# Kernel optimization log

Hardware: AMD Instinct MI355X
Metric: run time of the kernel (lower is better)

## Reference

```python
import jax, jax.numpy as jnp
from jax import lax
import numpy as np

EPS = 1e-5  # BatchNorm eps


def setup_inputs() -> dict:
    key = jax.random.key(0)
    ks = jax.random.split(key, 4)
    T, B, C = 256, 128, 1024
    L, H, NCLS = 6, 1024, 1000
    x = jax.random.normal(ks[0], (T, B, C), dtype=jnp.float32)
    W = jax.random.normal(ks[1], (L, C, H), dtype=jnp.float32) * (1.0 / np.sqrt(C))
    b = jnp.zeros((L, H), dtype=jnp.float32)
    gamma = jnp.ones((L, H), dtype=jnp.float32)
    beta = jnp.zeros((L, H), dtype=jnp.float32)
    u = jax.random.uniform(ks[2], (L, H), dtype=jnp.float32)  # recurrent weights in (0, U_bound~1)
    Wc = jax.random.normal(ks[3], (H, NCLS), dtype=jnp.float32) * (1.0 / np.sqrt(H))
    bc = jnp.zeros((NCLS,), dtype=jnp.float32)
    return {"x": x, "W": W, "b": b, "gamma": gamma, "beta": beta, "u": u, "Wc": Wc, "bc": bc}


def _layer(h, Wl, bl, gl, betal, ul):
    # per-timestep dense projection: [T,B,Cin] @ [Cin,H]
    z = jnp.einsum('tbi,ih->tbh', h, Wl) + bl
    # BN over (time, batch) per channel (bn_before, training-mode batch stats)
    mean = jnp.mean(z, axis=(0, 1))
    var = jnp.var(z, axis=(0, 1))
    z = (z - mean) * (gl / jnp.sqrt(var + EPS)) + betal
    # IndRNN diagonal recurrence: h_t = relu(z_t + u * h_{t-1}), h_0 = 0
    T, B, H = z.shape
    def step(hprev, zt):
        hnew = jax.nn.relu(zt + ul * hprev)
        return hnew, hnew
    _, hs = lax.scan(step, jnp.zeros((B, H), dtype=z.dtype), z)
    return hs


def reference(x, W, b, gamma, beta, u, Wc, bc):
    h = x
    for l in range(W.shape[0]):
        h = _layer(h, W[l], b[l], gamma[l], beta[l], u[l])
    # classifier on last timestep
    return h[-1] @ Wc + bc
```

## Files before the change

### kernel.cpp

```cpp
#include <hip/hip_runtime.h>
#include <hip/hip_bf16.h>

#define T_DIM 256
#define B_DIM 128
#define C_DIM 1024
#define H_DIM 1024
#define L_DIM 6
#define NC_DIM 1000
#define M_DIM (T_DIM * B_DIM)
#define BH_DIM (B_DIM * H_DIM)

typedef __attribute__((ext_vector_type(8))) short bf16x8;
typedef __attribute__((ext_vector_type(4))) float f32x4;

__device__ __forceinline__ float bf2f(unsigned short u) {
  union { unsigned int i; float f; } v; v.i = ((unsigned int)u) << 16; return v.f;
}
__device__ __forceinline__ unsigned short f2bf(float f) {
  union { float f; unsigned int i; } v; v.f = f;
  unsigned int r = v.i + 0x7fffu + ((v.i >> 16) & 1u);
  return (unsigned short)(r >> 16);
}
__device__ __forceinline__ unsigned int pack2bf(float lo, float hi) {
  __hip_bfloat162 b2 = __float22bfloat162_rn(float2{lo, hi});
  union { __hip_bfloat162 b; unsigned int u; } cv; cv.b = b2; return cv.u;
}

__device__ __forceinline__ void gload_lds16(const void* g, void* l) {
  __builtin_amdgcn_global_load_lds(
      (const __attribute__((address_space(1))) unsigned int*)g,
      (__attribute__((address_space(3))) unsigned int*)l, 16, 0, 0);
}

__global__ __launch_bounds__(256) void f32_to_bf16_kernel(
    const float* __restrict__ in, unsigned short* __restrict__ out, int n4) {
  int stride = gridDim.x * blockDim.x;
  for (int i = blockIdx.x * blockDim.x + threadIdx.x; i < n4; i += stride) {
    float4 v = ((const float4*)in)[i];
    unsigned int lo = pack2bf(v.x, v.y);
    unsigned int hi = pack2bf(v.z, v.w);
    uint2 o; o.x = lo; o.y = hi;
    ((uint2*)out)[i] = o;
  }
}

__global__ __launch_bounds__(256) void wtrans_kernel(
    const float* __restrict__ W, unsigned short* __restrict__ Wt) {
  __shared__ float tile[32][33];
  int l = blockIdx.z;
  const float* Wl = W + (size_t)l * C_DIM * H_DIM;
  unsigned short* Wtl = Wt + (size_t)l * C_DIM * H_DIM;
  int h0 = blockIdx.x * 32, c0 = blockIdx.y * 32;
  int tx = threadIdx.x, ty = threadIdx.y;
#pragma unroll
  for (int i = 0; i < 32; i += 8)
    tile[ty + i][tx] = Wl[(size_t)(c0 + ty + i) * H_DIM + h0 + tx];
  __syncthreads();
#pragma unroll
  for (int i = 0; i < 32; i += 8)
    Wtl[(size_t)(h0 + ty + i) * C_DIM + c0 + tx] = f2bf(tile[tx][ty + i]);
}

#define NT 32

__global__ __launch_bounds__(512, 2) void gemm_kernel(
    const unsigned short* __restrict__ A, const unsigned short* __restrict__ Bt,
    unsigned short* __restrict__ Z, float* __restrict__ psum, float* __restrict__ psqs) {
  extern __shared__ char lds[];
  int bid = blockIdx.x;
  int swz = (bid & 7) * 32 + (bid >> 3);
  int tm0 = (swz >> 2) * 2;
  int tn = swz & 3;
  int tid = threadIdx.x;
  int wv = tid >> 6, ln = tid & 63;
  int wm = wv >> 2, wn = wv & 3;

  const char* Ap0 = (const char*)A + (size_t)tm0 * 256 * 2048;
  const char* Ap1 = Ap0 + (size_t)256 * 2048;
  const char* Bpanel = (const char*)Bt + (size_t)tn * 256 * 2048;

  int p0 = wv * 1024 + ln * 16;
  int l0 = p0 ^ (((p0 >> 7) & 3) << 4);
  size_t ro0 = (size_t)(p0 >> 6) * 2048 + (l0 & 63);
  size_t ro1 = (size_t)(128 + (p0 >> 6)) * 2048 + (l0 & 63);
  int sdst = wv * 1024;

  auto stage = [&](const char* Ap, int t) {
    char* base = lds + ((t & 3) * 32768);
    int kb = t * 64;
    gload_lds16(Ap + ro0 + kb, base + sdst);
    gload_lds16(Ap + ro1 + kb, base + 8192 + sdst);
    gload_lds16(Bpanel + ro0 + kb, base + 16384 + sdst);
    gload_lds16(Bpanel + ro1 + kb, base + 16384 + 8192 + sdst);
  };

  int frow = ln & 15;
  int fchunk = ((ln >> 4) ^ (frow >> 1)) & 3;
  int floff = frow * 64 + (fchunk << 4);

  f32x4 acc[8][4];

  bf16x8 bX[4], aP[4], aQ[4];
  auto readB_to = [&](int t, bf16x8* d) {
    const char* Bb = lds + ((t & 3) * 32768) + 16384 + wn * 4096;
#pragma unroll
    for (int n = 0; n < 4; ++n) d[n] = *(const bf16x8*)(Bb + n * 1024 + floff);
  };
  auto readA_to = [&](int t, int mq, bf16x8* d) {
    const char* Ab = lds + ((t & 3) * 32768) + wm * 8192 + mq * 4096;
#pragma unroll
    for (int i = 0; i < 4; ++i) d[i] = *(const bf16x8*)(Ab + i * 1024 + floff);
  };

  auto kloop = [&](const char* Ap) {
    f32x4 zero = {0.f, 0.f, 0.f, 0.f};
#pragma unroll
    for (int m = 0; m < 8; ++m)
#pragma unroll
      for (int n = 0; n < 4; ++n) acc[m][n] = zero;
    readB_to(0, bX); readA_to(0, 0, aP);
    for (int t = 0; t < NT; ++t) {
      readA_to(t, 1, aQ);
      if (t <= NT - 4) stage(Ap, t + 3);
      __builtin_amdgcn_s_setprio(1);
#pragma unroll
      for (int i = 0; i < 4; ++i)
#pragma unroll
        for (int n = 0; n < 4; ++n)
          acc[i][n] = __builtin_amdgcn_mfma_f32_16x16x32_bf16(aP[i], bX[n], acc[i][n], 0, 0, 0);
      __builtin_amdgcn_s_setprio(0);
      __builtin_amdgcn_s_setprio(1);
#pragma unroll
      for (int i = 0; i < 4; ++i)
#pragma unroll
        for (int n = 0; n < 4; ++n)
          acc[4 + i][n] = __builtin_amdgcn_mfma_f32_16x16x32_bf16(aQ[i], bX[n], acc[4 + i][n], 0, 0, 0);
      __builtin_amdgcn_s_setprio(0);
      if (t < NT - 1) {
        readB_to(t + 1, bX); readA_to(t + 1, 0, aP);
        if (t <= NT - 4) { asm volatile("s_waitcnt vmcnt(4)" ::: "memory"); }
        else             { asm volatile("s_waitcnt vmcnt(0)" ::: "memory"); }
        __builtin_amdgcn_s_barrier();
      }
    }
  };

  float* red = (float*)(lds + 3 * 32768);
  auto epilogue = [&](int tm) {
    float s[4], q[4];
#pragma unroll
    for (int n = 0; n < 4; ++n) {
      float sv = 0.f, qv = 0.f;
#pragma unroll
      for (int m = 0; m < 8; ++m)
#pragma unroll
        for (int r = 0; r < 4; ++r) {
          float v = acc[m][n][r];
          sv += v; qv += v * v;
        }
      s[n] = sv; q[n] = qv;
    }
#pragma unroll
    for (int n = 0; n < 4; ++n) {
      s[n] += __shfl_xor(s[n], 16); s[n] += __shfl_xor(s[n], 32);
      q[n] += __shfl_xor(q[n], 16); q[n] += __shfl_xor(q[n], 32);
    }
    if (ln < 16) {
#pragma unroll
      for (int n = 0; n < 4; ++n) {
        red[wm * 256 + wn * 64 + n * 16 + ln] = s[n];
        red[512 + wm * 256 + wn * 64 + n * 16 + ln] = q[n];
      }
    }
    __syncthreads();
    if (tid < 256) {
      psum[(size_t)tm * H_DIM + tn * 256 + tid] = red[tid] + red[256 + tid];
    } else {
      int c = tid - 256;
      psqs[(size_t)tm * H_DIM + tn * 256 + c] = red[512 + c] + red[768 + c];
    }
    __syncthreads();
    int r0 = tm * 256 + wm * 128 + ((ln >> 4) << 2);
    int c0 = tn * 256 + wn * 64 + (ln & 15);
#pragma unroll
    for (int m = 0; m < 8; ++m)
#pragma unroll
      for (int n = 0; n < 4; ++n) {
        unsigned short* zp = Z + (size_t)(r0 + m * 16) * H_DIM + c0 + n * 16;
#pragma unroll
        for (int r = 0; r < 4; ++r) zp[(size_t)r * H_DIM] = f2bf(acc[m][n][r]);
      }
  };

  stage(Ap0, 0); stage(Ap0, 1); stage(Ap0, 2);
  asm volatile("s_waitcnt vmcnt(4)" ::: "memory");
  __builtin_amdgcn_s_barrier();
  kloop(Ap0);
  __builtin_amdgcn_s_barrier();
  stage(Ap1, 0); stage(Ap1, 1); stage(Ap1, 2);
  epilogue(tm0);
  asm volatile("s_waitcnt vmcnt(4)" ::: "memory");
  __builtin_amdgcn_s_barrier();
  kloop(Ap1);
  __builtin_amdgcn_s_barrier();
  epilogue(tm0 + 1);
}

__global__ __launch_bounds__(256) void bn_finalize_kernel(
    const float* __restrict__ psum, const float* __restrict__ psqs,
    const float* __restrict__ gamma, const float* __restrict__ beta,
    float* __restrict__ ss) {
  int c = blockIdx.x * blockDim.x + threadIdx.x;
  float s = 0.f, q = 0.f;
#pragma unroll 8
  for (int i = 0; i < 128; ++i) {
    s += psum[(size_t)i * H_DIM + c];
    q += psqs[(size_t)i * H_DIM + c];
  }
  const float invN = 1.0f / (float)M_DIM;
  float mean = s * invN;
  float var = q * invN - mean * mean;
  float sc = gamma[c] * rsqrtf(var + 1e-5f);
  ss[c] = sc;
  ss[H_DIM + c] = beta[c] - mean * sc;
}

__global__ __launch_bounds__(256) void bn_recur_kernel(
    const unsigned short* __restrict__ Z, const float* __restrict__ ss,
    const float* __restrict__ u, unsigned short* __restrict__ Hout) {
  int i2 = blockIdx.x * 256 + threadIdx.x;
  int h0 = (i2 & (H_DIM / 2 - 1)) * 2;
  float sc0 = ss[h0], sc1 = ss[h0 + 1];
  float sh0 = ss[H_DIM + h0], sh1 = ss[H_DIM + h0 + 1];
  float u0 = u[h0], u1 = u[h0 + 1];
  float hv0 = 0.f, hv1 = 0.f;

  const size_t ST = BH_DIM / 2;
  const unsigned int* Zt = (const unsigned int*)Z + i2;
  unsigned int* Ht = (unsigned int*)Hout + i2;

  unsigned int za[32], zb[32], ho[32];
#pragma unroll
  for (int j = 0; j < 32; ++j) za[j] = Zt[(size_t)j * ST];

#pragma unroll
  for (int blk = 0; blk < 4; ++blk) {
    int tA = blk * 64;
#pragma unroll
    for (int j = 0; j < 32; ++j) zb[j] = Zt[(size_t)(tA + 32 + j) * ST];
#pragma unroll
    for (int j = 0; j < 32; ++j) {
      unsigned int zz = za[j];
      float z0 = fmaf(bf2f((unsigned short)(zz & 0xffffu)), sc0, sh0);
      float z1 = fmaf(bf2f((unsigned short)(zz >> 16)), sc1, sh1);
      hv0 = fmaxf(fmaf(u0, hv0, z0), 0.f);
      hv1 = fmaxf(fmaf(u1, hv1, z1), 0.f);
      ho[j] = pack2bf(hv0, hv1);
    }
#pragma unroll
    for (int j = 0; j < 32; ++j) Ht[(size_t)(tA + j) * ST] = ho[j];
    if (blk < 3) {
#pragma unroll
      for (int j = 0; j < 32; ++j) za[j] = Zt[(size_t)(tA + 64 + j) * ST];
    }
#pragma unroll
    for (int j = 0; j < 32; ++j) {
      unsigned int zz = zb[j];
      float z0 = fmaf(bf2f((unsigned short)(zz & 0xffffu)), sc0, sh0);
      float z1 = fmaf(bf2f((unsigned short)(zz >> 16)), sc1, sh1);
      hv0 = fmaxf(fmaf(u0, hv0, z0), 0.f);
      hv1 = fmaxf(fmaf(u1, hv1, z1), 0.f);
      ho[j] = pack2bf(hv0, hv1);
    }
#pragma unroll
    for (int j = 0; j < 32; ++j) Ht[(size_t)(tA + 32 + j) * ST] = ho[j];
  }
}

__global__ __launch_bounds__(256) void classifier_kernel(
    const unsigned short* __restrict__ hlast, const float* __restrict__ Wc,
    const float* __restrict__ bc, float* __restrict__ out) {
  __shared__ float hs[H_DIM];
  int b = blockIdx.y;
  int n = blockIdx.x * 256 + threadIdx.x;
  for (int k = threadIdx.x; k < H_DIM; k += 256)
    hs[k] = bf2f(hlast[(size_t)b * H_DIM + k]);
  __syncthreads();
  if (n < NC_DIM) {
    float acc = bc[n];
#pragma unroll 8
    for (int k = 0; k < H_DIM; ++k)
      acc = fmaf(hs[k], Wc[(size_t)k * NC_DIM + n], acc);
    out[(size_t)b * NC_DIM + n] = acc;
  }
}

extern "C" void kernel_launch(void* const* d_in, const int* in_sizes, int n_in,
                              void* d_out, int out_size, void* d_ws, size_t ws_size,
                              hipStream_t stream) {
  const float* x     = (const float*)d_in[0];
  const float* W     = (const float*)d_in[1];
  const float* gamma = (const float*)d_in[3];
  const float* beta  = (const float*)d_in[4];
  const float* u     = (const float*)d_in[5];
  const float* Wc    = (const float*)d_in[6];
  const float* bc    = (const float*)d_in[7];
  float* out = (float*)d_out;

  const size_t CH = (size_t)C_DIM * H_DIM;
  const size_t MH = (size_t)M_DIM * H_DIM;
  char* p = (char*)d_ws;
  unsigned short* Wt = (unsigned short*)p; p += L_DIM * CH * sizeof(unsigned short);
  unsigned short* Ha = (unsigned short*)p; p += MH * sizeof(unsigned short);
  unsigned short* Hb = (unsigned short*)p; p += MH * sizeof(unsigned short);
  unsigned short* Z  = (unsigned short*)p; p += MH * sizeof(unsigned short);
  float* psum = (float*)p; p += 128 * H_DIM * sizeof(float);
  float* psqs = (float*)p; p += 128 * H_DIM * sizeof(float);
  float* ss   = (float*)p; p += 2 * H_DIM * sizeof(float);

  f32_to_bf16_kernel<<<2048, 256, 0, stream>>>(x, Ha, (int)(MH / 4));
  wtrans_kernel<<<dim3(H_DIM / 32, C_DIM / 32, L_DIM), dim3(32, 8), 0, stream>>>(W, Wt);

  unsigned short* cur = Ha;
  unsigned short* nxt = Hb;
  for (int l = 0; l < L_DIM; ++l) {
    gemm_kernel<<<256, 512, 131072, stream>>>(cur, Wt + (size_t)l * CH, Z, psum, psqs);
    bn_finalize_kernel<<<4, 256, 0, stream>>>(psum, psqs, gamma + (size_t)l * H_DIM,
                                              beta + (size_t)l * H_DIM, ss);
    bn_recur_kernel<<<BH_DIM / 512, 256, 0, stream>>>(Z, ss, u + (size_t)l * H_DIM, nxt);
    unsigned short* tmp = cur; cur = nxt; nxt = tmp;
  }
  classifier_kernel<<<dim3(4, B_DIM), 256, 0, stream>>>(
      cur + (size_t)(T_DIM - 1) * BH_DIM, Wc, bc, out);
}
```

Before: 769.7 us.

## Stage BN-recurrence input through LDS with async loads and skip unused last-layer writes

The BN+IndRNN recurrence kernel now double-buffers Z tiles of 32 timesteps into shared memory using global_load_lds. It computes the recurrence from LDS, stages outputs in LDS, and writes them back as coalesced 16-byte stores. In the final layer only the last timestep is stored, since the classifier reads nothing else. The change targets the latency-bound strided per-thread register loads of the old version. In exchange it uses 96KB of LDS per block, which limits occupancy, and adds barriers between chunks.

```diff
diff --git a/kernel.cpp b/kernel.cpp
--- a/kernel.cpp
+++ b/kernel.cpp
@@ -37,9 +37,7 @@
   int stride = gridDim.x * blockDim.x;
   for (int i = blockIdx.x * blockDim.x + threadIdx.x; i < n4; i += stride) {
     float4 v = ((const float4*)in)[i];
-    unsigned int lo = pack2bf(v.x, v.y);
-    unsigned int hi = pack2bf(v.z, v.w);
-    uint2 o; o.x = lo; o.y = hi;
+    uint2 o; o.x = pack2bf(v.x, v.y); o.y = pack2bf(v.z, v.w);
     ((uint2*)out)[i] = o;
   }
 }
@@ -227,53 +225,67 @@
 
 __global__ __launch_bounds__(256) void bn_recur_kernel(
     const unsigned short* __restrict__ Z, const float* __restrict__ ss,
-    const float* __restrict__ u, unsigned short* __restrict__ Hout) {
-  int i2 = blockIdx.x * 256 + threadIdx.x;
-  int h0 = (i2 & (H_DIM / 2 - 1)) * 2;
+    const float* __restrict__ u, unsigned short* __restrict__ Hout, int full) {
+  __shared__ char sbuf[98304];
+  char* in0 = sbuf;
+  char* in1 = sbuf + 32768;
+  char* outb = sbuf + 65536;
+  int blk = blockIdx.x;
+  int tid = threadIdx.x;
+  int wv = tid >> 6, ln = tid & 63;
+
+  int h0 = ((blk * 256 + tid) & (H_DIM / 2 - 1)) * 2;
   float sc0 = ss[h0], sc1 = ss[h0 + 1];
   float sh0 = ss[H_DIM + h0], sh1 = ss[H_DIM + h0 + 1];
   float u0 = u[h0], u1 = u[h0 + 1];
   float hv0 = 0.f, hv1 = 0.f;
 
-  const size_t ST = BH_DIM / 2;
-  const unsigned int* Zt = (const unsigned int*)Z + i2;
-  unsigned int* Ht = (unsigned int*)Hout + i2;
-
-  unsigned int za[32], zb[32], ho[32];
-#pragma unroll
-  for (int j = 0; j < 32; ++j) za[j] = Zt[(size_t)j * ST];
-
-#pragma unroll
-  for (int blk = 0; blk < 4; ++blk) {
-    int tA = blk * 64;
-#pragma unroll
-    for (int j = 0; j < 32; ++j) zb[j] = Zt[(size_t)(tA + 32 + j) * ST];
-#pragma unroll
-    for (int j = 0; j < 32; ++j) {
-      unsigned int zz = za[j];
+  const char* Zb = (const char*)Z + (size_t)blk * 1024;
+  char* Hb = (char*)Hout + (size_t)blk * 1024;
+  const size_t ROWB = (size_t)BH_DIM * 2;
+
+  auto stage = [&](int c) {
+    char* dst = (c & 1) ? in1 : in0;
+    int t0 = c * 32;
+#pragma unroll
+    for (int j = 0; j < 8; ++j) {
+      int r = wv * 8 + j;
+      gload_lds16(Zb + (size_t)(t0 + r) * ROWB + ln * 16, dst + r * 1024);
+    }
+  };
+
+  stage(0);
+  asm volatile("s_waitcnt vmcnt(0)" ::: "memory");
+  __builtin_amdgcn_s_barrier();
+
+  for (int c = 0; c < 8; ++c) {
+    if (c < 7) stage(c + 1);
+    const char* inb = (c & 1) ? in1 : in0;
+#pragma unroll
+    for (int t = 0; t < 32; ++t) {
+      unsigned int zz = *(const unsigned int*)(inb + t * 1024 + tid * 4);
       float z0 = fmaf(bf2f((unsigned short)(zz & 0xffffu)), sc0, sh0);
       float z1 = fmaf(bf2f((unsigned short)(zz >> 16)), sc1, sh1);
       hv0 = fmaxf(fmaf(u0, hv0, z0), 0.f);
       hv1 = fmaxf(fmaf(u1, hv1, z1), 0.f);
-      ho[j] = pack2bf(hv0, hv1);
-    }
-#pragma unroll
-    for (int j = 0; j < 32; ++j) Ht[(size_t)(tA + j) * ST] = ho[j];
-    if (blk < 3) {
-#pragma unroll
-      for (int j = 0; j < 32; ++j) za[j] = Zt[(size_t)(tA + 64 + j) * ST];
-    }
-#pragma unroll
-    for (int j = 0; j < 32; ++j) {
-      unsigned int zz = zb[j];
-      float z0 = fmaf(bf2f((unsigned short)(zz & 0xffffu)), sc0, sh0);
-      float z1 = fmaf(bf2f((unsigned short)(zz >> 16)), sc1, sh1);
-      hv0 = fmaxf(fmaf(u0, hv0, z0), 0.f);
-      hv1 = fmaxf(fmaf(u1, hv1, z1), 0.f);
-      ho[j] = pack2bf(hv0, hv1);
-    }
-#pragma unroll
-    for (int j = 0; j < 32; ++j) Ht[(size_t)(tA + 32 + j) * ST] = ho[j];
+      *(unsigned int*)(outb + t * 1024 + tid * 4) = pack2bf(hv0, hv1);
+    }
+    asm volatile("s_waitcnt lgkmcnt(0)" ::: "memory");
+    __builtin_amdgcn_s_barrier();
+    int t0 = c * 32;
+#pragma unroll
+    for (int j = 0; j < 8; ++j) {
+      int r = wv * 8 + j;
+      if (full || (c == 7 && r == 31)) {
+        uint4 v = *(const uint4*)(outb + r * 1024 + ln * 16);
+        *(uint4*)(Hb + (size_t)(t0 + r) * ROWB + ln * 16) = v;
+      }
+    }
+    if (c < 7) {
+      if (full) { asm volatile("s_waitcnt lgkmcnt(0) vmcnt(8)" ::: "memory"); }
+      else      { asm volatile("s_waitcnt lgkmcnt(0) vmcnt(0)" ::: "memory"); }
+      __builtin_amdgcn_s_barrier();
+    }
   }
 }
 
@@ -327,7 +339,8 @@
     gemm_kernel<<<256, 512, 131072, stream>>>(cur, Wt + (size_t)l * CH, Z, psum, psqs);
     bn_finalize_kernel<<<4, 256, 0, stream>>>(psum, psqs, gamma + (size_t)l * H_DIM,
                                               beta + (size_t)l * H_DIM, ss);
-    bn_recur_kernel<<<BH_DIM / 512, 256, 0, stream>>>(Z, ss, u + (size_t)l * H_DIM, nxt);
+    bn_recur_kernel<<<256, 256, 0, stream>>>(Z, ss, u + (size_t)l * H_DIM, nxt,
+                                             (l < L_DIM - 1) ? 1 : 0);
     unsigned short* tmp = cur; cur = nxt; nxt = tmp;
   }
   classifier_kernel<<<dim3(4, B_DIM), 256, 0, stream>>>(
```

New measurement: 815.5 us. 1.06x slower.
